# Optimization experiments

Hardware: AMD Instinct MI355X
Metric: run time of the kernel (lower is better)

## Reference

```python
import jax, jax.numpy as jnp
import numpy as np

D_MODEL = 1024
N_HEADS = 16
HEAD_DIM = D_MODEL // N_HEADS


def setup_inputs() -> dict:
    key = jax.random.key(0)
    ks = jax.random.split(key, 5)
    B, T = 2, 2048
    x = jax.random.normal(ks[0], (B, T, D_MODEL), dtype=jnp.float32)
    s_in = 1.0 / np.sqrt(D_MODEL)
    W_qkv = jax.random.normal(ks[1], (D_MODEL, 3 * D_MODEL), dtype=jnp.float32) * s_in
    b_qkv = jnp.zeros((3 * D_MODEL,), dtype=jnp.float32)
    W_out = jax.random.normal(ks[2], (D_MODEL, D_MODEL), dtype=jnp.float32) * s_in
    b_out = jnp.zeros((D_MODEL,), dtype=jnp.float32)
    gamma = jnp.ones((D_MODEL,), dtype=jnp.float32)
    beta = jnp.zeros((D_MODEL,), dtype=jnp.float32)
    return {"x": x, "W_qkv": W_qkv, "b_qkv": b_qkv, "W_out": W_out,
            "b_out": b_out, "gamma": gamma, "beta": beta}


def _layernorm(x, gamma, beta, eps=1e-5):
    mu = jnp.mean(x, axis=-1, keepdims=True)
    var = jnp.var(x, axis=-1, keepdims=True)
    return (x - mu) * jax.lax.rsqrt(var + eps) * gamma + beta


def reference(x, W_qkv, b_qkv, W_out, b_out, gamma, beta):
    B, T, D = x.shape
    residual = x
    h = _layernorm(x, gamma, beta)
    qkv = h @ W_qkv + b_qkv                      # [B, T, 3D]
    qkv = qkv.reshape(B, T, 3, N_HEADS, HEAD_DIM)
    q = jnp.transpose(qkv[:, :, 0], (0, 2, 1, 3))  # [B, H, T, hd]
    k = jnp.transpose(qkv[:, :, 1], (0, 2, 1, 3))
    v = jnp.transpose(qkv[:, :, 2], (0, 2, 1, 3))
    scale = 1.0 / np.sqrt(HEAD_DIM)
    attn = jnp.einsum("bhqd,bhkd->bhqk", q, k) * scale
    attn = jax.nn.softmax(attn, axis=-1)
    out = jnp.einsum("bhqk,bhkd->bhqd", attn, v)   # [B, H, T, hd]
    out = jnp.transpose(out, (0, 2, 1, 3)).reshape(B, T, D)
    out = out @ W_out + b_out
    return residual + out
```

## Files before the change

### kernel.cpp

```cpp
#include <hip/hip_runtime.h>
#include <hip/hip_bf16.h>


#define DINL static __device__ __forceinline__

typedef __attribute__((ext_vector_type(8))) short bf16x8;
typedef __attribute__((ext_vector_type(4))) float f32x4;

DINL float fast_exp2(float x) { return __builtin_amdgcn_exp2f(x); }

DINL unsigned short f2bf(float f) {
  __hip_bfloat16 h = __float2bfloat16(f);
  unsigned short u;
  __builtin_memcpy(&u, &h, 2);
  return u;
}

DINL unsigned int bfbits(float f) {
  unsigned int u;
  __builtin_memcpy(&u, &f, 4);
  return (u + 0x8000u) >> 16;
}

DINL void gload_lds16(const void* g, void* l) {
  __builtin_amdgcn_global_load_lds((__attribute__((address_space(1))) void*)g,
                                   (__attribute__((address_space(3))) void*)l,
                                   16, 0, 0);
}

__global__ __launch_bounds__(256)
void ln_kernel(const float* __restrict__ x, const float* __restrict__ gamma,
               const float* __restrict__ beta, unsigned short* __restrict__ h) {
  __shared__ float red[8];
  int row = blockIdx.x;
  int t = threadIdx.x;
  float4 v = reinterpret_cast<const float4*>(x + (size_t)row * 1024)[t];
  float s  = v.x + v.y + v.z + v.w;
  float sq = v.x*v.x + v.y*v.y + v.z*v.z + v.w*v.w;
#pragma unroll
  for (int off = 1; off < 64; off <<= 1) {
    s  += __shfl_xor(s, off);
    sq += __shfl_xor(sq, off);
  }
  int wid = t >> 6;
  if ((t & 63) == 0) { red[wid] = s; red[4 + wid] = sq; }
  __syncthreads();
  s  = red[0] + red[1] + red[2] + red[3];
  sq = red[4] + red[5] + red[6] + red[7];
  float mu   = s * (1.0f / 1024.0f);
  float var  = sq * (1.0f / 1024.0f) - mu * mu;
  float rstd = rsqrtf(var + 1e-5f);
  float4 g = reinterpret_cast<const float4*>(gamma)[t];
  float4 b = reinterpret_cast<const float4*>(beta)[t];
  ushort4 o;
  o.x = f2bf((v.x - mu) * rstd * g.x + b.x);
  o.y = f2bf((v.y - mu) * rstd * g.y + b.y);
  o.z = f2bf((v.z - mu) * rstd * g.z + b.z);
  o.w = f2bf((v.w - mu) * rstd * g.w + b.w);
  reinterpret_cast<ushort4*>(h + (size_t)row * 1024)[t] = o;
}

__global__ __launch_bounds__(256)
void transpose_cast_kernel(const float* __restrict__ src, unsigned short* __restrict__ dst,
                           int R, int C) {
  __shared__ float tile[32][33];
  int tx = threadIdx.x & 31, ty = threadIdx.x >> 5;
  int c0 = blockIdx.x * 32, r0 = blockIdx.y * 32;
#pragma unroll
  for (int i = 0; i < 4; i++)
    tile[ty + i * 8][tx] = src[(size_t)(r0 + ty + i * 8) * C + c0 + tx];
  __syncthreads();
#pragma unroll
  for (int i = 0; i < 4; i++) {
    int r = ty + i * 8;
    dst[(size_t)(c0 + r) * R + r0 + tx] = f2bf(tile[tx][r]);
  }
}

template <int BM, int MODE>
__global__ __launch_bounds__(256)
void gemm128(const unsigned short* __restrict__ A,
             const unsigned short* __restrict__ Bt,
             int K,
             const float* __restrict__ bias,
             unsigned short* __restrict__ qdst, unsigned short* __restrict__ kdst,
             unsigned short* __restrict__ vTdst,
             const float* __restrict__ xres, float* __restrict__ out) {
  static_assert(BM == 128 || BM == 64, "");
  constexpr int MR = BM / 32;
  __shared__ unsigned short As[BM * 64];
  __shared__ unsigned short Bs[8192];
  int tid = threadIdx.x, wid = tid >> 6, lane = tid & 63;
  int l15 = lane & 15, l4 = lane >> 4;
  int brow = blockIdx.y * BM, bcol = blockIdx.x * 128;
  int wr = wid >> 1, wc = wid & 1;
  f32x4 acc[MR][4] = {};

  for (int kt = 0; kt < K; kt += 64) {
    __syncthreads();
#pragma unroll
    for (int r = 0; r < MR; r++) {
      int c  = wid * (BM * 2) + r * 64;
      int cl = c + lane;
      int kb = cl / BM, row = cl % BM;
      gload_lds16(A + (size_t)(brow + row) * K + kt + kb * 8, As + c * 8);
    }
#pragma unroll
    for (int r = 0; r < 4; r++) {
      int c  = wid * 256 + r * 64;
      int cl = c + lane;
      int kb = cl >> 7, row = cl & 127;
      gload_lds16(Bt + (size_t)(bcol + row) * K + kt + kb * 8, Bs + c * 8);
    }
    __syncthreads();
#pragma unroll
    for (int ks = 0; ks < 2; ks++) {
      int kb = ks * 4 + l4;
      bf16x8 af[MR], bfr[4];
#pragma unroll
      for (int m = 0; m < MR; m++)
        af[m] = *reinterpret_cast<const bf16x8*>(As + (kb * BM + wr * (BM / 2) + m * 16 + l15) * 8);
#pragma unroll
      for (int n = 0; n < 4; n++)
        bfr[n] = *reinterpret_cast<const bf16x8*>(Bs + (kb * 128 + wc * 64 + n * 16 + l15) * 8);
#pragma unroll
      for (int m = 0; m < MR; m++)
#pragma unroll
        for (int n = 0; n < 4; n++)
          acc[m][n] = __builtin_amdgcn_mfma_f32_16x16x32_bf16(af[m], bfr[n], acc[m][n], 0, 0, 0);
    }
  }

  if (MODE == 0) {
    int sec = bcol >> 10;
    int secbase = sec << 10;
#pragma unroll
    for (int m = 0; m < MR; m++) {
      int row0 = brow + wr * (BM / 2) + m * 16 + l4 * 4;
      int b = row0 >> 11, t0 = row0 & 2047;
#pragma unroll
      for (int n = 0; n < 4; n++) {
        int col = (bcol & 1023) + wc * 64 + n * 16 + l15;
        float bv = bias[secbase + col];
        int hh = col >> 6, d = col & 63;
        if (sec == 2) {
          ushort4 pk;
          pk.x = f2bf(acc[m][n][0] + bv);
          pk.y = f2bf(acc[m][n][1] + bv);
          pk.z = f2bf(acc[m][n][2] + bv);
          pk.w = f2bf(acc[m][n][3] + bv);
          *reinterpret_cast<ushort4*>(vTdst + ((size_t)(b * 16 + hh) * 64 + d) * 2048 + t0) = pk;
        } else {
          unsigned short* dst = (sec == 0) ? qdst : kdst;
          float sc = (sec == 0) ? 0.125f * 1.44269504088896f : 1.0f;
#pragma unroll
          for (int j = 0; j < 4; j++)
            dst[((size_t)(b * 16 + hh) * 2048 + t0 + j) * 64 + d] = f2bf((acc[m][n][j] + bv) * sc);
        }
      }
    }
  } else {
#pragma unroll
    for (int m = 0; m < MR; m++) {
      int row0 = brow + wr * (BM / 2) + m * 16 + l4 * 4;
#pragma unroll
      for (int n = 0; n < 4; n++) {
        int col = bcol + wc * 64 + n * 16 + l15;
        float bv = bias[col];
#pragma unroll
        for (int j = 0; j < 4; j++) {
          size_t idx = (size_t)(row0 + j) * 1024 + col;
          out[idx] = acc[m][n][j] + bv + xres[idx];
        }
      }
    }
  }
}

__global__ __launch_bounds__(256, 2)
void attn_kernel(const unsigned short* __restrict__ q,
                 const unsigned short* __restrict__ kk,
                 const unsigned short* __restrict__ vT,
                 unsigned short* __restrict__ o) {
  const int T = 2048;
  __shared__ unsigned short Ks[2][16384];
  __shared__ unsigned short Ps[4][2048];
  int tid = threadIdx.x, wid = tid >> 6, lane = tid & 63;
  int l15 = lane & 15, l4 = lane >> 4;
  int swz = (l15 & 7) << 3;

  int lin = blockIdx.x;
  int rl  = (lin & 7) * 64 + (lin >> 3);
  int bx = rl & 15, bh = rl >> 4;
  int q0 = bx * 128 + wid * 32;

  const unsigned short* qh = q  + (size_t)bh * T * 64;
  const unsigned short* kh = kk + (size_t)bh * T * 64;
  const unsigned short* vh = vT + (size_t)bh * 64 * T;

  bf16x8 qf[2][2];
#pragma unroll
  for (int m = 0; m < 2; m++)
#pragma unroll
    for (int ks = 0; ks < 2; ks++)
      qf[m][ks] = *reinterpret_cast<const bf16x8*>(
          qh + (size_t)(q0 + m * 16 + l15) * 64 + ks * 32 + l4 * 8);

  f32x4 accO[2][4] = {};
  float lst[2] = {0.0f, 0.0f};

#define STAGE256(buf, kv0)                                                     \
  {                                                                            \
    _Pragma("unroll") for (int r = 0; r < 8; r++) {                            \
      int c  = (wid * 8 + r) * 64;                                             \
      int cl = c + lane;                                                       \
      int key = cl >> 3;                                                       \
      int kb  = (cl & 7) ^ (key & 7);                                          \
      gload_lds16(kh + (size_t)((kv0) + key) * 64 + kb * 8, &Ks[buf][c * 8]);  \
    }                                                                          \
  }

#define SUBTILE(sub, vf)                                                       \
  {                                                                            \
    f32x4 s[2][4] = {};                                                        \
    __builtin_amdgcn_s_setprio(1);                                             \
    _Pragma("unroll") for (int ks = 0; ks < 2; ks++) {                         \
      _Pragma("unroll") for (int n = 0; n < 4; n++) {                          \
        int kkey = (sub) * 64 + n * 16 + l15;                                  \
        int slot = kkey * 8 + ((ks * 4 + l4) ^ (kkey & 7));                    \
        bf16x8 kf = *reinterpret_cast<const bf16x8*>(&Ks[cur][slot * 8]);      \
        _Pragma("unroll") for (int m = 0; m < 2; m++)                          \
          s[m][n] = __builtin_amdgcn_mfma_f32_16x16x32_bf16(kf, qf[m][ks],     \
                                                            s[m][n], 0, 0, 0); \
      }                                                                        \
    }                                                                          \
    __builtin_amdgcn_s_setprio(0);                                             \
    _Pragma("unroll") for (int m = 0; m < 2; m++) {                            \
      float sum = 0.0f;                                                        \
      _Pragma("unroll") for (int n = 0; n < 4; n++) {                          \
        _Pragma("unroll") for (int j = 0; j < 4; j++) {                        \
          float p = fast_exp2(s[m][n][j]);                                     \
          s[m][n][j] = p;                                                      \
          sum += p;                                                            \
        }                                                                      \
        unsigned int u0 = bfbits(s[m][n][0]) | (bfbits(s[m][n][1]) << 16);     \
        unsigned int u1 = bfbits(s[m][n][2]) | (bfbits(s[m][n][3]) << 16);     \
        *reinterpret_cast<uint2*>(                                             \
            &Ps[wid][(m * 16 + l15) * 64 + ((n * 16 + l4 * 4) ^ swz)]) =       \
            make_uint2(u0, u1);                                                \
      }                                                                        \
      lst[m] += sum;                                                           \
    }                                                                          \
    _Pragma("unroll") for (int ks = 0; ks < 2; ks++) {                         \
      _Pragma("unroll") for (int m = 0; m < 2; m++) {                          \
        bf16x8 pf = *reinterpret_cast<const bf16x8*>(                          \
            &Ps[wid][(m * 16 + l15) * 64 + ((ks * 32 + l4 * 8) ^ swz)]);       \
        __builtin_amdgcn_s_setprio(1);                                         \
        _Pragma("unroll") for (int n = 0; n < 4; n++)                          \
          accO[m][n] = __builtin_amdgcn_mfma_f32_16x16x32_bf16(                \
              vf[ks][n], pf, accO[m][n], 0, 0, 0);                             \
        __builtin_amdgcn_s_setprio(0);                                         \
      }                                                                        \
    }                                                                          \
  }

#define LOADV(vf, kvs)                                                         \
  {                                                                            \
    _Pragma("unroll") for (int ks = 0; ks < 2; ks++)                           \
      _Pragma("unroll") for (int n = 0; n < 4; n++)                            \
        vf[ks][n] = *reinterpret_cast<const bf16x8*>(                          \
            vh + (size_t)(n * 16 + l15) * T + (kvs) + ks * 32 + l4 * 8);       \
  }

  STAGE256(0, 0);
  __syncthreads();
  int cur = 0;

  for (int kv0 = 0; kv0 < T; kv0 += 256) {
    bf16x8 vf0[2][4];
    LOADV(vf0, kv0);
    if (kv0 + 256 < T) STAGE256(cur ^ 1, kv0 + 256);
    SUBTILE(0, vf0);
    bf16x8 vf1[2][4];
    LOADV(vf1, kv0 + 64);
    SUBTILE(1, vf1);
    bf16x8 vf2[2][4];
    LOADV(vf2, kv0 + 128);
    SUBTILE(2, vf2);
    bf16x8 vf3[2][4];
    LOADV(vf3, kv0 + 192);
    SUBTILE(3, vf3);
    __syncthreads();
    cur ^= 1;
  }
#undef SUBTILE
#undef LOADV
#undef STAGE256

  int b = bh >> 4, hh = bh & 15;
#pragma unroll
  for (int m = 0; m < 2; m++) {
    float l = lst[m];
    l += __shfl_xor(l, 16);
    l += __shfl_xor(l, 32);
    float inv = 1.0f / l;
    int row = q0 + m * 16 + l15;
#pragma unroll
    for (int n = 0; n < 4; n++) {
      ushort4 pk;
      pk.x = f2bf(accO[m][n][0] * inv);
      pk.y = f2bf(accO[m][n][1] * inv);
      pk.z = f2bf(accO[m][n][2] * inv);
      pk.w = f2bf(accO[m][n][3] * inv);
      *reinterpret_cast<ushort4*>(
          &o[(size_t)(b * 2048 + row) * 1024 + hh * 64 + n * 16 + l4 * 4]) = pk;
    }
  }
}

extern "C" void kernel_launch(void* const* d_in, const int* in_sizes, int n_in,
                              void* d_out, int out_size, void* d_ws, size_t ws_size,
                              hipStream_t stream) {
  const float* x     = (const float*)d_in[0];
  const float* W_qkv = (const float*)d_in[1];
  const float* b_qkv = (const float*)d_in[2];
  const float* W_out = (const float*)d_in[3];
  const float* b_out = (const float*)d_in[4];
  const float* gamma = (const float*)d_in[5];
  const float* beta  = (const float*)d_in[6];
  float* out = (float*)d_out;

  char* ws = (char*)d_ws;
  unsigned short* h     = (unsigned short*)(ws);
  unsigned short* WqkvT = (unsigned short*)(ws + (size_t)(8)  * 1024 * 1024);
  unsigned short* WoutT = (unsigned short*)(ws + (size_t)(14) * 1024 * 1024);
  unsigned short* qb    = (unsigned short*)(ws + (size_t)(16) * 1024 * 1024);
  unsigned short* kb    = (unsigned short*)(ws + (size_t)(24) * 1024 * 1024);
  unsigned short* vTb   = (unsigned short*)(ws + (size_t)(32) * 1024 * 1024);
  unsigned short* attno = (unsigned short*)(ws + (size_t)(40) * 1024 * 1024);

  ln_kernel<<<4096, 256, 0, stream>>>(x, gamma, beta, h);
  transpose_cast_kernel<<<dim3(96, 32), 256, 0, stream>>>(W_qkv, WqkvT, 1024, 3072);
  transpose_cast_kernel<<<dim3(32, 32), 256, 0, stream>>>(W_out, WoutT, 1024, 1024);
  gemm128<128, 0><<<dim3(24, 32), 256, 0, stream>>>(h, WqkvT, 1024, b_qkv, qb, kb, vTb, nullptr, nullptr);
  attn_kernel<<<512, 256, 0, stream>>>(qb, kb, vTb, attno);
  gemm128<64, 1><<<dim3(8, 64), 256, 0, stream>>>(attno, WoutT, 1024, b_out, nullptr, nullptr, nullptr, x, out);
}
```

Before: 169.2 us.

## Shrink K stage to 128 keys and batch QK/softmax before PV per iteration

The attention loop now stages 128 keys of K per LDS buffer instead of 256, and each iteration processes two 64-key subtiles. Both QK^T+exp subtiles run first into double-buffered per-wave P tiles, then both PV MFMA blocks run, with V fragments for both subtiles loaded up front. This is meant to give the scheduler more independent MFMA and exp work to interleave and to hide V global-load latency. In exchange the loop synchronises twice as often, and more registers are held for V fragments, which may pressure occupancy.

```diff
diff --git a/kernel.cpp b/kernel.cpp
--- a/kernel.cpp
+++ b/kernel.cpp
@@ -183,8 +183,8 @@
                  const unsigned short* __restrict__ vT,
                  unsigned short* __restrict__ o) {
   const int T = 2048;
-  __shared__ unsigned short Ks[2][16384];
-  __shared__ unsigned short Ps[4][2048];
+  __shared__ unsigned short Ks[2][8192];
+  __shared__ unsigned short Ps[4][2][2048];
   int tid = threadIdx.x, wid = tid >> 6, lane = tid & 63;
   int l15 = lane & 15, l4 = lane >> 4;
   int swz = (l15 & 7) << 3;
@@ -209,10 +209,10 @@
   f32x4 accO[2][4] = {};
   float lst[2] = {0.0f, 0.0f};
 
-#define STAGE256(buf, kv0)                                                     \
+#define STAGE128(buf, kv0)                                                     \
   {                                                                            \
-    _Pragma("unroll") for (int r = 0; r < 8; r++) {                            \
-      int c  = (wid * 8 + r) * 64;                                             \
+    _Pragma("unroll") for (int r = 0; r < 4; r++) {                            \
+      int c  = (wid * 4 + r) * 64;                                             \
       int cl = c + lane;                                                       \
       int key = cl >> 3;                                                       \
       int kb  = (cl & 7) ^ (key & 7);                                          \
@@ -220,7 +220,7 @@
     }                                                                          \
   }
 
-#define SUBTILE(sub, vf)                                                       \
+#define QKSM(sub, par)                                                         \
   {                                                                            \
     f32x4 s[2][4] = {};                                                        \
     __builtin_amdgcn_s_setprio(1);                                             \
@@ -246,22 +246,26 @@
         unsigned int u0 = bfbits(s[m][n][0]) | (bfbits(s[m][n][1]) << 16);     \
         unsigned int u1 = bfbits(s[m][n][2]) | (bfbits(s[m][n][3]) << 16);     \
         *reinterpret_cast<uint2*>(                                             \
-            &Ps[wid][(m * 16 + l15) * 64 + ((n * 16 + l4 * 4) ^ swz)]) =       \
+            &Ps[wid][par][(m * 16 + l15) * 64 + ((n * 16 + l4 * 4) ^ swz)]) =  \
             make_uint2(u0, u1);                                                \
       }                                                                        \
       lst[m] += sum;                                                           \
     }                                                                          \
+  }
+
+#define PV(par, vf)                                                            \
+  {                                                                            \
+    __builtin_amdgcn_s_setprio(1);                                             \
     _Pragma("unroll") for (int ks = 0; ks < 2; ks++) {                         \
       _Pragma("unroll") for (int m = 0; m < 2; m++) {                          \
         bf16x8 pf = *reinterpret_cast<const bf16x8*>(                          \
-            &Ps[wid][(m * 16 + l15) * 64 + ((ks * 32 + l4 * 8) ^ swz)]);       \
-        __builtin_amdgcn_s_setprio(1);                                         \
+            &Ps[wid][par][(m * 16 + l15) * 64 + ((ks * 32 + l4 * 8) ^ swz)]);  \
         _Pragma("unroll") for (int n = 0; n < 4; n++)                          \
           accO[m][n] = __builtin_amdgcn_mfma_f32_16x16x32_bf16(                \
               vf[ks][n], pf, accO[m][n], 0, 0, 0);                             \
-        __builtin_amdgcn_s_setprio(0);                                         \
       }                                                                        \
     }                                                                          \
+    __builtin_amdgcn_s_setprio(0);                                             \
   }
 
 #define LOADV(vf, kvs)                                                         \
@@ -272,30 +276,26 @@
             vh + (size_t)(n * 16 + l15) * T + (kvs) + ks * 32 + l4 * 8);       \
   }
 
-  STAGE256(0, 0);
+  STAGE128(0, 0);
   __syncthreads();
   int cur = 0;
 
-  for (int kv0 = 0; kv0 < T; kv0 += 256) {
-    bf16x8 vf0[2][4];
+  for (int kv0 = 0; kv0 < T; kv0 += 128) {
+    bf16x8 vf0[2][4], vf1[2][4];
     LOADV(vf0, kv0);
-    if (kv0 + 256 < T) STAGE256(cur ^ 1, kv0 + 256);
-    SUBTILE(0, vf0);
-    bf16x8 vf1[2][4];
     LOADV(vf1, kv0 + 64);
-    SUBTILE(1, vf1);
-    bf16x8 vf2[2][4];
-    LOADV(vf2, kv0 + 128);
-    SUBTILE(2, vf2);
-    bf16x8 vf3[2][4];
-    LOADV(vf3, kv0 + 192);
-    SUBTILE(3, vf3);
+    if (kv0 + 128 < T) STAGE128(cur ^ 1, kv0 + 128);
+    QKSM(0, 0);
+    QKSM(1, 1);
+    PV(0, vf0);
+    PV(1, vf1);
     __syncthreads();
     cur ^= 1;
   }
-#undef SUBTILE
+#undef QKSM
+#undef PV
 #undef LOADV
-#undef STAGE256
+#undef STAGE128
 
   int b = bh >> 4, hh = bh & 15;
 #pragma unroll
```

Result: no change. 167.8 us (-0.9%).
